# Kernel tuning notes

Measured on AMD Instinct MI355X. Metric: run time of the kernel, lower is better.

Reference implementation:

```python
import jax, jax.numpy as jnp
import numpy as np

NOISE_STD = 0.001


def setup_inputs() -> dict:
    key = jax.random.key(0)
    k1, k2, k3, k4 = jax.random.split(key, 4)
    B, T, NIN, NREC = 64, 2048, 64, 1024
    x = jax.random.normal(k1, (B, T, NIN), dtype=jnp.float32)
    W_ih = jax.random.normal(k2, (NREC, NIN), dtype=jnp.float32) / np.sqrt(NIN)
    W_hh = jax.random.normal(k3, (NREC, NREC), dtype=jnp.float32) / np.sqrt(NREC)
    noise = jax.random.normal(k4, (T, NREC), dtype=jnp.float32)
    return {"x": x, "W_ih": W_ih, "W_hh": W_hh, "noise": noise}


def reference(x, W_ih, W_hh, noise):
    # x: [B, T, n_in] -> scan over time (strict sequential dependency)
    B = x.shape[0]
    NREC = W_hh.shape[0]
    x_t = jnp.transpose(x, (1, 0, 2))            # [T, B, n_in]
    xproj = jnp.einsum('tbi,ri->tbr', x_t, W_ih)  # hoist input GEMM out of scan
    noise_scaled = noise * NOISE_STD              # [T, NREC], broadcast over batch
    h0 = jnp.zeros((B, NREC), dtype=x.dtype)

    def step(h_prev, inp):
        xp, n_t = inp
        h = xp + jnp.tanh(h_prev) @ W_hh.T + n_t[None, :]
        return h, h[-1]  # original appends h_t[-1] (last batch element)

    h_last, outs = jax.lax.scan(step, h0, (xproj, noise_scaled))
    output = outs.T  # stack -> [T, NREC], transpose(0,1) -> [NREC, T]
    return output, h_last
```

## Files before the change

kernel.cpp:

```cpp
#include <hip/hip_runtime.h>


#define TT    2048
#define BB    64
#define NIN   64
#define NRECN 1024
#define KTOT  1088
#define NGRP  8
#define WPGRP 16
#define NWG   128
#define NOISE_STD 0.001f

typedef __attribute__((ext_vector_type(8))) _Float16 half8;
typedef __attribute__((ext_vector_type(4))) float f32x4;
typedef __attribute__((ext_vector_type(2))) unsigned int u32x2;

__device__ __forceinline__ void st_d2_sc1(void* p, u32x2 w) {
  asm volatile("global_store_dwordx2 %0, %1, off sc1" :: "v"(p), "v"(w) : "memory");
}
__device__ __forceinline__ unsigned pk2h(float a, float b) {
  unsigned short ua = __builtin_bit_cast(unsigned short, (_Float16)a);
  unsigned short ub = __builtin_bit_cast(unsigned short, (_Float16)b);
  return (unsigned)ua | ((unsigned)ub << 16);
}
__device__ __forceinline__ half8 cvt8(const f32x4& a, const f32x4& b) {
  half8 r;
  #pragma unroll
  for (int j = 0; j < 4; ++j) { r[j] = (_Float16)a[j]; r[4+j] = (_Float16)b[j]; }
  return r;
}

#define LDA16(V, P, OFF) \
  asm volatile("global_load_dwordx4 %0, %1, off offset:%c2" \
               : "=&v"(V) : "v"(P), "n"(OFF))
#define WAITV(N) asm volatile("s_waitcnt vmcnt(" #N ")" ::: "memory")
#define SB0 __builtin_amdgcn_sched_barrier(0)
#define MFMA16 __builtin_amdgcn_mfma_f32_16x16x32_f16

#define ACHUNK(c) {                                            \
    half8 b0 = *(const half8*)(whp0 + (c) * 2048);             \
    half8 b1 = *(const half8*)(whp1 + (c) * 2048);             \
    if ((c) & 1) {                                             \
      Q0 = MFMA16(b0, A[c], Q0, 0, 0, 0);                      \
      Q1 = MFMA16(b1, A[c], Q1, 0, 0, 0);                      \
    } else {                                                   \
      P0 = MFMA16(b0, A[c], P0, 0, 0, 0);                      \
      P1 = MFMA16(b1, A[c], P1, 0, 0, 0);                      \
    } }

__global__ __launch_bounds__(128, 1) void rnn_scan_kernel(
    const float* __restrict__ x, const float* __restrict__ W_ih,
    const float* __restrict__ W_hh, const float* __restrict__ noise,
    float* __restrict__ out, int* __restrict__ flags,
    _Float16* __restrict__ th)
{
  extern __shared__ _Float16 smem[];

  const int wg = blockIdx.x, grp = wg & 7, gidx = wg >> 3;
  const int tid = threadIdx.x, lane = tid & 63, wv = tid >> 6;
  const int l15 = lane & 15, g4 = lane >> 4;

  for (int idx = tid; idx < 64 * KTOT; idx += 128) {
    int nr = idx / KTOT, k = idx - nr * KTOT;
    int ng = gidx * 64 + nr;
    float v = (k < NRECN) ? W_hh[(size_t)ng * NRECN + k]
                          : W_ih[(size_t)ng * NIN + (k - NRECN)];
    smem[(k >> 3) * 512 + nr * 8 + (k & 7)] = (_Float16)v;
  }
  __syncthreads();

  int* ctr = flags + grp * 16;
  const _Float16* whp0 = smem + g4 * 512 + (wv * 32 + l15) * 8;
  const _Float16* whp1 = whp0 + 128;
  _Float16* thg = th + grp * (2 * 8 * 1024);
  const int b_eff = grp * 8 + (l15 & 7);
  const float* xrow = x + (size_t)b_eff * TT * NIN;
  const int cB = gidx * 64 + wv * 32 + g4 * 4;

  f32x4 xv0, xv1, xv2, xv3, nv0, nv1;
  { const float* xp = xrow + g4 * 8;
    xv0 = *(const f32x4*)xp;        xv1 = *(const f32x4*)(xp + 4);
    xv2 = *(const f32x4*)(xp + 32); xv3 = *(const f32x4*)(xp + 36);
    nv0 = *(const f32x4*)(noise + cB);
    nv1 = *(const f32x4*)(noise + cB + 16); }

  for (int t = 0; t < TT; ++t) {
    f32x4 P0{0,0,0,0}, P1{0,0,0,0}, Q0{0,0,0,0}, Q1{0,0,0,0};

    if (t > 0) {
      const int target = t * WPGRP;
      if (tid == 0) {
        while (__hip_atomic_load(ctr, __ATOMIC_RELAXED,
                                 __HIP_MEMORY_SCOPE_AGENT) < target) { }
      }
      if (wv == 0)
        __builtin_amdgcn_fence(__ATOMIC_ACQUIRE, "agent");
      __syncthreads();

      const _Float16* abase =
          thg + (t & 1) * 8192 + (l15 & 7) * 1024 + g4 * 8;
      half8 A[32];
      #pragma unroll
      for (int c = 0; c < 8; ++c)  LDA16(A[c], abase, c * 64);
      #pragma unroll
      for (int c = 8; c < 16; ++c) LDA16(A[c], abase, c * 64);
      WAITV(8);  SB0;
      #pragma unroll
      for (int c = 16; c < 24; ++c) LDA16(A[c], abase, c * 64);
      #pragma unroll
      for (int c = 0; c < 8; ++c)  ACHUNK(c);
      WAITV(8);  SB0;
      #pragma unroll
      for (int c = 24; c < 32; ++c) LDA16(A[c], abase, c * 64);
      #pragma unroll
      for (int c = 8; c < 16; ++c) ACHUNK(c);
      WAITV(8);  SB0;
      #pragma unroll
      for (int c = 16; c < 24; ++c) ACHUNK(c);
      WAITV(0);  SB0;
      #pragma unroll
      for (int c = 24; c < 32; ++c) ACHUNK(c);
    }

    {
      half8 xh0 = cvt8(xv0, xv1), xh1 = cvt8(xv2, xv3);
      half8 b0 = *(const half8*)(whp0 + 32 * 2048);
      half8 b1 = *(const half8*)(whp1 + 32 * 2048);
      P0 = MFMA16(b0, xh0, P0, 0, 0, 0);
      P1 = MFMA16(b1, xh0, P1, 0, 0, 0);
      b0 = *(const half8*)(whp0 + 33 * 2048);
      b1 = *(const half8*)(whp1 + 33 * 2048);
      P0 = MFMA16(b0, xh1, P0, 0, 0, 0);
      P1 = MFMA16(b1, xh1, P1, 0, 0, 0);
    }

    f32x4 y0, y1, y2, y3, m0, m1;
    {
      const int tt = (t + 1 < TT) ? t + 1 : t;
      const float* xp = xrow + (size_t)tt * NIN + g4 * 8;
      const float* np = noise + (size_t)tt * NRECN + cB;
      LDA16(y0, xp, 0);   LDA16(y1, xp, 16);
      LDA16(y2, xp, 128); LDA16(y3, xp, 144);
      LDA16(m0, np, 0);   LDA16(m1, np, 64);
    }

    f32x4 h0, h1;
    #pragma unroll
    for (int r = 0; r < 4; ++r) {
      h0[r] = P0[r] + Q0[r] + nv0[r] * NOISE_STD;
      h1[r] = P1[r] + Q1[r] + nv1[r] * NOISE_STD;
    }
    _Float16* ob = thg + ((t + 1) & 1) * 8192;
    float tv0[4], tv1[4];
    #pragma unroll
    for (int r = 0; r < 4; ++r) {
      tv0[r] = 1.f - 2.f / (__expf(2.f * h0[r]) + 1.f);
      tv1[r] = 1.f - 2.f / (__expf(2.f * h1[r]) + 1.f);
    }
    if (l15 < 8) {
      u32x2 w0, w1;
      w0[0] = pk2h(tv0[0], tv0[1]); w0[1] = pk2h(tv0[2], tv0[3]);
      w1[0] = pk2h(tv1[0], tv1[1]); w1[1] = pk2h(tv1[2], tv1[3]);
      st_d2_sc1(ob + l15 * 1024 + cB, w0);
      st_d2_sc1(ob + l15 * 1024 + cB + 16, w1);
    }
    WAITV(0);
    __syncthreads();
    if (tid == 0)
      __hip_atomic_fetch_add(ctr, 1, __ATOMIC_RELAXED,
                             __HIP_MEMORY_SCOPE_AGENT);

    xv0 = y0; xv1 = y1; xv2 = y2; xv3 = y3; nv0 = m0; nv1 = m1;

    if (grp == 7 && l15 == 7) {
      #pragma unroll
      for (int r = 0; r < 4; ++r) {
        out[(size_t)(cB + r) * TT + t] = h0[r];
        out[(size_t)(cB + 16 + r) * TT + t] = h1[r];
      }
    }
    if (t == TT - 1 && l15 < 8) {
      const int br = grp * 8 + l15;
      *(f32x4*)(out + (size_t)NRECN * TT + (size_t)br * NRECN + cB) = h0;
      *(f32x4*)(out + (size_t)NRECN * TT + (size_t)br * NRECN + cB + 16) = h1;
    }
  }
}

extern "C" void kernel_launch(void* const* d_in, const int* in_sizes, int n_in,
                              void* d_out, int out_size, void* d_ws, size_t ws_size,
                              hipStream_t stream) {
  const float* x     = (const float*)d_in[0];
  const float* W_ih  = (const float*)d_in[1];
  const float* W_hh  = (const float*)d_in[2];
  const float* noise = (const float*)d_in[3];
  float* out = (float*)d_out;

  char* ws = (char*)d_ws;
  int* flags = (int*)ws;
  _Float16* th = (_Float16*)(ws + 4096);

  (void)hipMemsetAsync(flags, 0, 4096, stream);

  const size_t lds_bytes = (size_t)136 * 64 * 8 * sizeof(_Float16);
  (void)hipFuncSetAttribute((const void*)rnn_scan_kernel,
                            hipFuncAttributeMaxDynamicSharedMemorySize,
                            (int)lds_bytes);

  rnn_scan_kernel<<<dim3(NWG), dim3(128), lds_bytes, stream>>>(
      x, W_ih, W_hh, noise, out, flags, th);
}
```

Baseline: 10.10 ms.

## Process all 64 batch rows per workgroup with 16 workgroups and triple-buffered loads

Cuts the grid from 128 workgroups (8 batch groups of 8 rows × 16 column slices) to 16 workgroups that each handle all 64 batch rows for a 64-column slice. Each wave now runs 4× more MFMAs per weight load and uses all 16 MFMA rows instead of half. Synchronisation changes from one shared counter per batch group to per-workgroup flags that 16 lanes poll. Hidden-state loads use a 3-slot rotating pipeline. Fewer workgroups means less inter-CU sync traffic per step, but each step does more serial work on one CU and needs more registers.

```diff
diff --git a/kernel.cpp b/kernel.cpp
--- a/kernel.cpp
+++ b/kernel.cpp
@@ -6,9 +6,7 @@
 #define NIN   64
 #define NRECN 1024
 #define KTOT  1088
-#define NGRP  8
-#define WPGRP 16
-#define NWG   128
+#define NWG   16
 #define NOISE_STD 0.001f
 
 typedef __attribute__((ext_vector_type(8))) _Float16 half8;
@@ -37,16 +35,29 @@
 #define SB0 __builtin_amdgcn_sched_barrier(0)
 #define MFMA16 __builtin_amdgcn_mfma_f32_16x16x32_f16
 
-#define ACHUNK(c) {                                            \
-    half8 b0 = *(const half8*)(whp0 + (c) * 2048);             \
-    half8 b1 = *(const half8*)(whp1 + (c) * 2048);             \
-    if ((c) & 1) {                                             \
-      Q0 = MFMA16(b0, A[c], Q0, 0, 0, 0);                      \
-      Q1 = MFMA16(b1, A[c], Q1, 0, 0, 0);                      \
-    } else {                                                   \
-      P0 = MFMA16(b0, A[c], P0, 0, 0, 0);                      \
-      P1 = MFMA16(b1, A[c], P1, 0, 0, 0);                      \
-    } }
+#define ISSUE(b, s) do {                                           \
+    _Pragma("unroll")                                              \
+    for (int m_ = 0; m_ < 4; ++m_) {                               \
+      LDA16(A[s][0 * 4 + m_], ab[m_], (2 * (b)) * 64);             \
+      LDA16(A[s][1 * 4 + m_], ab[m_], (2 * (b) + 1) * 64);         \
+    } } while (0)
+
+#define COMPUTE(b, s) do {                                         \
+    _Pragma("unroll")                                              \
+    for (int i2_ = 0; i2_ < 2; ++i2_) {                            \
+      const int c_ = 2 * (b) + i2_;                                \
+      half8 w0_ = *(const half8*)(whp0 + c_ * 2048);               \
+      half8 w1_ = *(const half8*)(whp1 + c_ * 2048);               \
+      _Pragma("unroll")                                            \
+      for (int m_ = 0; m_ < 4; ++m_) {                             \
+        acc0[m_] = MFMA16(w0_, A[s][i2_ * 4 + m_], acc0[m_], 0, 0, 0); \
+        acc1[m_] = MFMA16(w1_, A[s][i2_ * 4 + m_], acc1[m_], 0, 0, 0); \
+      } } } while (0)
+
+#define STEPB(b, WN) do {                                          \
+    WAITV(WN); SB0;                                                \
+    if ((b) + 2 < 16) ISSUE((b) + 2, ((b) + 2) % 3);               \
+    COMPUTE(b, (b) % 3); } while (0)
 
 __global__ __launch_bounds__(128, 1) void rnn_scan_kernel(
     const float* __restrict__ x, const float* __restrict__ W_ih,
@@ -56,133 +67,141 @@
 {
   extern __shared__ _Float16 smem[];
 
-  const int wg = blockIdx.x, grp = wg & 7, gidx = wg >> 3;
+  const int wg = blockIdx.x;
   const int tid = threadIdx.x, lane = tid & 63, wv = tid >> 6;
   const int l15 = lane & 15, g4 = lane >> 4;
 
   for (int idx = tid; idx < 64 * KTOT; idx += 128) {
     int nr = idx / KTOT, k = idx - nr * KTOT;
-    int ng = gidx * 64 + nr;
+    int ng = wg * 64 + nr;
     float v = (k < NRECN) ? W_hh[(size_t)ng * NRECN + k]
                           : W_ih[(size_t)ng * NIN + (k - NRECN)];
     smem[(k >> 3) * 512 + nr * 8 + (k & 7)] = (_Float16)v;
   }
   __syncthreads();
 
-  int* ctr = flags + grp * 16;
   const _Float16* whp0 = smem + g4 * 512 + (wv * 32 + l15) * 8;
   const _Float16* whp1 = whp0 + 128;
-  _Float16* thg = th + grp * (2 * 8 * 1024);
-  const int b_eff = grp * 8 + (l15 & 7);
-  const float* xrow = x + (size_t)b_eff * TT * NIN;
-  const int cB = gidx * 64 + wv * 32 + g4 * 4;
-
-  f32x4 xv0, xv1, xv2, xv3, nv0, nv1;
-  { const float* xp = xrow + g4 * 8;
-    xv0 = *(const f32x4*)xp;        xv1 = *(const f32x4*)(xp + 4);
-    xv2 = *(const f32x4*)(xp + 32); xv3 = *(const f32x4*)(xp + 36);
-    nv0 = *(const f32x4*)(noise + cB);
-    nv1 = *(const f32x4*)(noise + cB + 16); }
+  const int cB = wg * 64 + wv * 32 + g4 * 4;
+
+  const float* xr[4];
+  #pragma unroll
+  for (int m = 0; m < 4; ++m)
+    xr[m] = x + (size_t)(m * 16 + l15) * TT * NIN + g4 * 8;
+
+  half8 xh0[4], xh1[4];
+  f32x4 nv0, nv1;
+  #pragma unroll
+  for (int m = 0; m < 4; ++m) {
+    xh0[m] = cvt8(*(const f32x4*)xr[m], *(const f32x4*)(xr[m] + 4));
+    xh1[m] = cvt8(*(const f32x4*)(xr[m] + 32), *(const f32x4*)(xr[m] + 36));
+  }
+  nv0 = *(const f32x4*)(noise + cB);
+  nv1 = *(const f32x4*)(noise + cB + 16);
 
   for (int t = 0; t < TT; ++t) {
-    f32x4 P0{0,0,0,0}, P1{0,0,0,0}, Q0{0,0,0,0}, Q1{0,0,0,0};
+    f32x4 acc0[4], acc1[4];
+    #pragma unroll
+    for (int m = 0; m < 4; ++m) {
+      acc0[m] = f32x4{0, 0, 0, 0}; acc1[m] = f32x4{0, 0, 0, 0};
+    }
 
     if (t > 0) {
-      const int target = t * WPGRP;
-      if (tid == 0) {
-        while (__hip_atomic_load(ctr, __ATOMIC_RELAXED,
-                                 __HIP_MEMORY_SCOPE_AGENT) < target) { }
+      if (wv == 0 && lane < NWG) {
+        while (__hip_atomic_load(&flags[lane * 16], __ATOMIC_RELAXED,
+                                 __HIP_MEMORY_SCOPE_AGENT) < t) { }
       }
       if (wv == 0)
         __builtin_amdgcn_fence(__ATOMIC_ACQUIRE, "agent");
       __syncthreads();
 
-      const _Float16* abase =
-          thg + (t & 1) * 8192 + (l15 & 7) * 1024 + g4 * 8;
-      half8 A[32];
-      #pragma unroll
-      for (int c = 0; c < 8; ++c)  LDA16(A[c], abase, c * 64);
-      #pragma unroll
-      for (int c = 8; c < 16; ++c) LDA16(A[c], abase, c * 64);
-      WAITV(8);  SB0;
-      #pragma unroll
-      for (int c = 16; c < 24; ++c) LDA16(A[c], abase, c * 64);
-      #pragma unroll
-      for (int c = 0; c < 8; ++c)  ACHUNK(c);
-      WAITV(8);  SB0;
-      #pragma unroll
-      for (int c = 24; c < 32; ++c) LDA16(A[c], abase, c * 64);
-      #pragma unroll
-      for (int c = 8; c < 16; ++c) ACHUNK(c);
-      WAITV(8);  SB0;
-      #pragma unroll
-      for (int c = 16; c < 24; ++c) ACHUNK(c);
-      WAITV(0);  SB0;
-      #pragma unroll
-      for (int c = 24; c < 32; ++c) ACHUNK(c);
+      const _Float16* ab[4];
+      #pragma unroll
+      for (int m = 0; m < 4; ++m)
+        ab[m] = th + (t & 1) * 65536 + (m * 16 + l15) * 1024 + g4 * 8;
+
+      half8 A[3][8];
+      ISSUE(0, 0); ISSUE(1, 1);
+      STEPB(0, 8);  STEPB(1, 8);  STEPB(2, 8);  STEPB(3, 8);
+      STEPB(4, 8);  STEPB(5, 8);  STEPB(6, 8);  STEPB(7, 8);
+      STEPB(8, 8);  STEPB(9, 8);  STEPB(10, 8); STEPB(11, 8);
+      STEPB(12, 8); STEPB(13, 8); STEPB(14, 8); STEPB(15, 0);
     }
 
     {
-      half8 xh0 = cvt8(xv0, xv1), xh1 = cvt8(xv2, xv3);
-      half8 b0 = *(const half8*)(whp0 + 32 * 2048);
-      half8 b1 = *(const half8*)(whp1 + 32 * 2048);
-      P0 = MFMA16(b0, xh0, P0, 0, 0, 0);
-      P1 = MFMA16(b1, xh0, P1, 0, 0, 0);
-      b0 = *(const half8*)(whp0 + 33 * 2048);
-      b1 = *(const half8*)(whp1 + 33 * 2048);
-      P0 = MFMA16(b0, xh1, P0, 0, 0, 0);
-      P1 = MFMA16(b1, xh1, P1, 0, 0, 0);
-    }
-
-    f32x4 y0, y1, y2, y3, m0, m1;
+      half8 wa0 = *(const half8*)(whp0 + 32 * 2048);
+      half8 wa1 = *(const half8*)(whp1 + 32 * 2048);
+      half8 wb0 = *(const half8*)(whp0 + 33 * 2048);
+      half8 wb1 = *(const half8*)(whp1 + 33 * 2048);
+      #pragma unroll
+      for (int m = 0; m < 4; ++m) {
+        acc0[m] = MFMA16(wa0, xh0[m], acc0[m], 0, 0, 0);
+        acc1[m] = MFMA16(wa1, xh0[m], acc1[m], 0, 0, 0);
+        acc0[m] = MFMA16(wb0, xh1[m], acc0[m], 0, 0, 0);
+        acc1[m] = MFMA16(wb1, xh1[m], acc1[m], 0, 0, 0);
+      }
+    }
+
+    f32x4 px[4][4], pn0, pn1;
     {
       const int tt = (t + 1 < TT) ? t + 1 : t;
-      const float* xp = xrow + (size_t)tt * NIN + g4 * 8;
+      #pragma unroll
+      for (int m = 0; m < 4; ++m) {
+        const float* xp = xr[m] + (size_t)tt * NIN;
+        LDA16(px[m][0], xp, 0);   LDA16(px[m][1], xp, 16);
+        LDA16(px[m][2], xp, 128); LDA16(px[m][3], xp, 144);
+      }
       const float* np = noise + (size_t)tt * NRECN + cB;
-      LDA16(y0, xp, 0);   LDA16(y1, xp, 16);
-      LDA16(y2, xp, 128); LDA16(y3, xp, 144);
-      LDA16(m0, np, 0);   LDA16(m1, np, 64);
-    }
-
-    f32x4 h0, h1;
+      LDA16(pn0, np, 0); LDA16(pn1, np, 64);
+    }
+
+    _Float16* ob = th + ((t + 1) & 1) * 65536;
+    f32x4 h0[4], h1[4];
     #pragma unroll
-    for (int r = 0; r < 4; ++r) {
-      h0[r] = P0[r] + Q0[r] + nv0[r] * NOISE_STD;
-      h1[r] = P1[r] + Q1[r] + nv1[r] * NOISE_STD;
-    }
-    _Float16* ob = thg + ((t + 1) & 1) * 8192;
-    float tv0[4], tv1[4];
-    #pragma unroll
-    for (int r = 0; r < 4; ++r) {
-      tv0[r] = 1.f - 2.f / (__expf(2.f * h0[r]) + 1.f);
-      tv1[r] = 1.f - 2.f / (__expf(2.f * h1[r]) + 1.f);
-    }
-    if (l15 < 8) {
+    for (int m = 0; m < 4; ++m) {
+      #pragma unroll
+      for (int r = 0; r < 4; ++r) {
+        h0[m][r] = acc0[m][r] + nv0[r] * NOISE_STD;
+        h1[m][r] = acc1[m][r] + nv1[r] * NOISE_STD;
+      }
+      float tv0[4], tv1[4];
+      #pragma unroll
+      for (int r = 0; r < 4; ++r) {
+        tv0[r] = 1.f - 2.f / (__expf(2.f * h0[m][r]) + 1.f);
+        tv1[r] = 1.f - 2.f / (__expf(2.f * h1[m][r]) + 1.f);
+      }
       u32x2 w0, w1;
       w0[0] = pk2h(tv0[0], tv0[1]); w0[1] = pk2h(tv0[2], tv0[3]);
       w1[0] = pk2h(tv1[0], tv1[1]); w1[1] = pk2h(tv1[2], tv1[3]);
-      st_d2_sc1(ob + l15 * 1024 + cB, w0);
-      st_d2_sc1(ob + l15 * 1024 + cB + 16, w1);
+      st_d2_sc1(ob + (m * 16 + l15) * 1024 + cB, w0);
+      st_d2_sc1(ob + (m * 16 + l15) * 1024 + cB + 16, w1);
     }
     WAITV(0);
+    #pragma unroll
+    for (int m = 0; m < 4; ++m) {
+      xh0[m] = cvt8(px[m][0], px[m][1]);
+      xh1[m] = cvt8(px[m][2], px[m][3]);
+    }
+    nv0 = pn0; nv1 = pn1;
     __syncthreads();
     if (tid == 0)
-      __hip_atomic_fetch_add(ctr, 1, __ATOMIC_RELAXED,
+      __hip_atomic_fetch_add(&flags[wg * 16], 1, __ATOMIC_RELAXED,
                              __HIP_MEMORY_SCOPE_AGENT);
 
-    xv0 = y0; xv1 = y1; xv2 = y2; xv3 = y3; nv0 = m0; nv1 = m1;
-
-    if (grp == 7 && l15 == 7) {
+    if (l15 == 15) {
       #pragma unroll
       for (int r = 0; r < 4; ++r) {
-        out[(size_t)(cB + r) * TT + t] = h0[r];
-        out[(size_t)(cB + 16 + r) * TT + t] = h1[r];
-      }
-    }
-    if (t == TT - 1 && l15 < 8) {
-      const int br = grp * 8 + l15;
-      *(f32x4*)(out + (size_t)NRECN * TT + (size_t)br * NRECN + cB) = h0;
-      *(f32x4*)(out + (size_t)NRECN * TT + (size_t)br * NRECN + cB + 16) = h1;
+        out[(size_t)(cB + r) * TT + t] = h0[3][r];
+        out[(size_t)(cB + 16 + r) * TT + t] = h1[3][r];
+      }
+    }
+    if (t == TT - 1) {
+      #pragma unroll
+      for (int m = 0; m < 4; ++m) {
+        const int br = m * 16 + l15;
+        *(f32x4*)(out + (size_t)NRECN * TT + (size_t)br * NRECN + cB) = h0[m];
+        *(f32x4*)(out + (size_t)NRECN * TT + (size_t)br * NRECN + cB + 16) = h1[m];
+      }
     }
   }
 }
```

New measurement: 22.41 ms. 122% more time.
